# Kernel tuning notes

Measured on AMD Instinct MI355X. Metric: run time of the kernel, lower is better.

Reference implementation:

```python
import jax, jax.numpy as jnp
import numpy as np

B, S, D = 2, 2048, 1024
H, DK, DV = 16, 64, 64
NEG = -1e9

def setup_inputs() -> dict:
    key = jax.random.key(0)
    ks = jax.random.split(key, 7)
    scale = 1.0 / np.sqrt(D)
    return {
        "Q": jax.random.normal(ks[0], (B, S, D), dtype=jnp.float32),
        "K": jax.random.normal(ks[1], (B, S, D), dtype=jnp.float32),
        "V": jax.random.normal(ks[2], (B, S, D), dtype=jnp.float32),
        "Wq": jax.random.normal(ks[3], (D, H * DK), dtype=jnp.float32) * scale,
        "Wk": jax.random.normal(ks[4], (D, H * DK), dtype=jnp.float32) * scale,
        "Wv": jax.random.normal(ks[5], (D, H * DV), dtype=jnp.float32) * scale,
        "Wo": jax.random.normal(ks[6], (H * DV, D), dtype=jnp.float32) * scale,
    }

def reference(Q, K, V, Wq, Wk, Wv, Wo):
    b, sq, _ = Q.shape
    sk = K.shape[1]
    # project and split heads: [b, h, s, d]
    q = (Q @ Wq).reshape(b, sq, H, DK).transpose(0, 2, 1, 3)
    k = (K @ Wk).reshape(b, sk, H, DK).transpose(0, 2, 1, 3)
    v = (V @ Wv).reshape(b, sk, H, DV).transpose(0, 2, 1, 3)
    scores = jnp.einsum("bhqd,bhkd->bhqk", q, k) / jnp.sqrt(jnp.float32(DK))
    causal = jnp.tril(jnp.ones((sq, sk), dtype=bool))
    scores = jnp.where(causal[None, None], scores, NEG)
    attn = jax.nn.softmax(scores, axis=-1)
    out = jnp.einsum("bhqk,bhkd->bhqd", attn, v)
    out = out.transpose(0, 2, 1, 3).reshape(b, sq, H * DV)
    return out @ Wo
```

## Files before the change

kernel.cpp:

```cpp
#include <hip/hip_runtime.h>
#include <cstdint>
#include <cstddef>


typedef __bf16 bf16x8 __attribute__((ext_vector_type(8)));
typedef __bf16 bf16x4 __attribute__((ext_vector_type(4)));
typedef float f32x4 __attribute__((ext_vector_type(4)));
typedef unsigned int u32x4 __attribute__((ext_vector_type(4)));

#define MFMA __builtin_amdgcn_mfma_f32_16x16x32_bf16

static __device__ __forceinline__ __bf16 f2b(float f) { return (__bf16)f; }

static __device__ __forceinline__ void gload_lds16(const void* g, void* l) {
  __builtin_amdgcn_global_load_lds(
      (const __attribute__((address_space(1))) void*)g,
      (__attribute__((address_space(3))) void*)l, 16, 0, 0);
}

#define QSCALE 0.18033688f

__global__ __launch_bounds__(256) void wtrans_kernel(
    const float* __restrict__ w0, const float* __restrict__ w1,
    const float* __restrict__ w2, const float* __restrict__ w3,
    __bf16* __restrict__ outT)
{
  const int z = blockIdx.z;
  const float* W = (z == 0) ? w0 : (z == 1) ? w1 : (z == 2) ? w2 : w3;
  __bf16* O = outT + (size_t)z * 1048576;
  __shared__ float t[32][33];
  const int tx = threadIdx.x & 31, ty = threadIdx.x >> 5;
  const int kb = blockIdx.y * 32, nb = blockIdx.x * 32;
#pragma unroll
  for (int i = 0; i < 4; i++)
    t[ty + i * 8][tx] = W[(size_t)(kb + ty + i * 8) * 1024 + nb + tx];
  __syncthreads();
#pragma unroll
  for (int i = 0; i < 4; i++)
    O[(size_t)(nb + ty + i * 8) * 1024 + kb + tx] = f2b(t[tx][ty + i * 8]);
}

__global__ __launch_bounds__(256) void cvt_kernel(
    const float* __restrict__ a0, const float* __restrict__ a1,
    const float* __restrict__ a2, __bf16* __restrict__ o0,
    __bf16* __restrict__ o1, __bf16* __restrict__ o2)
{
  const int z = blockIdx.y;
  const float* src = (z == 0) ? a0 : (z == 1) ? a1 : a2;
  __bf16* dst = (z == 0) ? o0 : (z == 1) ? o1 : o2;
  const int idx = blockIdx.x * 256 + threadIdx.x;
#pragma unroll
  for (int it = 0; it < 4; ++it) {
    const size_t c = (size_t)(idx + it * 131072) * 8;
    f32x4 v0 = *(const f32x4*)&src[c];
    f32x4 v1 = *(const f32x4*)&src[c + 4];
    bf16x8 w = {f2b(v0[0]), f2b(v0[1]), f2b(v0[2]), f2b(v0[3]),
                f2b(v1[0]), f2b(v1[1]), f2b(v1[2]), f2b(v1[3])};
    *(bf16x8*)&dst[c] = w;
  }
}

__global__ __launch_bounds__(256) void gemm_proj_bf16_kernel(
    const __bf16* __restrict__ A0, const __bf16* __restrict__ A1,
    const __bf16* __restrict__ A2, const __bf16* __restrict__ WT,
    __bf16* __restrict__ C0, __bf16* __restrict__ C1, __bf16* __restrict__ C2)
{
  const int z = blockIdx.y;
  const __bf16* A = (z == 0) ? A0 : (z == 1) ? A1 : A2;
  const __bf16* W = WT + (size_t)z * 1048576;
  __bf16* C = (z == 0) ? C0 : (z == 1) ? C1 : C2;
  const float osc = (z == 0) ? QSCALE : 1.0f;

  const int bid = blockIdx.x;
  const int t = (bid & 7) * 32 + (bid >> 3);
  const int mt = t >> 3, nt = t & 7;
  const int mbase = mt * 128, nbase = nt * 128;

  __shared__ __align__(16) __bf16 As[128][32];
  __shared__ __align__(16) __bf16 Bs[128][32];

  const int tid = threadIdx.x;
  const int wid = tid >> 6, lane = tid & 63;
  const int wr = wid >> 1, wc = wid & 1;
  const int lr = lane & 15, kg = lane >> 4;

  f32x4 acc[4][4] = {};

  const int srow = tid >> 2, scol = (tid & 3) * 8;
  const int wbase = tid & 192;

  for (int kb = 0; kb < 32; ++kb) {
    const int k0 = kb * 32;
    __syncthreads();
#pragma unroll
    for (int p = 0; p < 2; ++p) {
      const int r = srow + p * 64;
      gload_lds16(&A[(size_t)(mbase + r) * 1024 + k0 + scol],
                  (__bf16*)As + (size_t)(p * 256 + wbase) * 8);
      gload_lds16(&W[(size_t)(nbase + r) * 1024 + k0 + scol],
                  (__bf16*)Bs + (size_t)(p * 256 + wbase) * 8);
    }
    __syncthreads();

    bf16x8 af[4], bfr[4];
#pragma unroll
    for (int i = 0; i < 4; i++) af[i] = *(const bf16x8*)&As[wr * 64 + i * 16 + lr][kg * 8];
#pragma unroll
    for (int j = 0; j < 4; j++) bfr[j] = *(const bf16x8*)&Bs[wc * 64 + j * 16 + lr][kg * 8];
#pragma unroll
    for (int i = 0; i < 4; i++)
#pragma unroll
      for (int j = 0; j < 4; j++)
        acc[i][j] = MFMA(af[i], bfr[j], acc[i][j], 0, 0, 0);
  }

  if (z == 2) {
#pragma unroll
    for (int i = 0; i < 4; i++)
#pragma unroll
      for (int j = 0; j < 4; j++) {
        const int m0 = mbase + wr * 64 + i * 16 + kg * 4;
        const int n = nbase + wc * 64 + j * 16 + lr;
        const int b = m0 >> 11, s = m0 & 2047, h = n >> 6, dv = n & 63;
        bf16x4 w;
#pragma unroll
        for (int r = 0; r < 4; r++) w[r] = f2b(acc[i][j][r]);
        *(bf16x4*)&C[(((size_t)(b * 16 + h)) * 64 + dv) * 2048 + s] = w;
      }
  } else {
#pragma unroll
    for (int i = 0; i < 4; i++)
#pragma unroll
      for (int j = 0; j < 4; j++)
#pragma unroll
        for (int r = 0; r < 4; r++) {
          const int m = mbase + wr * 64 + i * 16 + kg * 4 + r;
          const int n = nbase + wc * 64 + j * 16 + lr;
          const int b = m >> 11, s = m & 2047, h = n >> 6, dk = n & 63;
          C[(((size_t)(b * 16 + h)) * 2048 + s) * 64 + dk] = f2b(acc[i][j][r] * osc);
        }
  }
}

__global__ __launch_bounds__(256) void gemm_proj_f32_kernel(
    const float* __restrict__ A0, const float* __restrict__ A1,
    const float* __restrict__ A2, const __bf16* __restrict__ WT,
    __bf16* __restrict__ C0, __bf16* __restrict__ C1, __bf16* __restrict__ C2)
{
  const int z = blockIdx.y;
  const float* A = (z == 0) ? A0 : (z == 1) ? A1 : A2;
  const __bf16* W = WT + (size_t)z * 1048576;
  __bf16* C = (z == 0) ? C0 : (z == 1) ? C1 : C2;
  const float osc = (z == 0) ? QSCALE : 1.0f;

  const int mt = blockIdx.x >> 3, nt = blockIdx.x & 7;
  const int mbase = mt * 128, nbase = nt * 128;

  __shared__ __align__(16) __bf16 As[128][40];
  __shared__ __align__(16) __bf16 Bs[128][40];

  const int tid = threadIdx.x;
  const int wid = tid >> 6, lane = tid & 63;
  const int wr = wid >> 1, wc = wid & 1;
  const int lr = lane & 15, kg = lane >> 4;

  f32x4 acc[4][4] = {};
  const int arow = tid >> 3, ac0 = (tid & 7) * 4;

  for (int kb = 0; kb < 32; ++kb) {
    const int k0 = kb * 32;
#pragma unroll
    for (int p = 0; p < 4; ++p) {
      const int r = arow + p * 32;
      f32x4 av = *(const f32x4*)&A[(size_t)(mbase + r) * 1024 + k0 + ac0];
      bf16x4 cv = {f2b(av[0]), f2b(av[1]), f2b(av[2]), f2b(av[3])};
      *(bf16x4*)&As[r][ac0] = cv;
    }
#pragma unroll
    for (int p = 0; p < 2; ++p) {
      const int idx = p * 256 + tid;
      const int r = idx >> 2, c8 = (idx & 3) * 8;
      *(u32x4*)&Bs[r][c8] = *(const u32x4*)&W[(size_t)(nbase + r) * 1024 + k0 + c8];
    }
    __syncthreads();

    bf16x8 af[4], bfr[4];
#pragma unroll
    for (int i = 0; i < 4; i++) af[i] = *(const bf16x8*)&As[wr * 64 + i * 16 + lr][kg * 8];
#pragma unroll
    for (int j = 0; j < 4; j++) bfr[j] = *(const bf16x8*)&Bs[wc * 64 + j * 16 + lr][kg * 8];
#pragma unroll
    for (int i = 0; i < 4; i++)
#pragma unroll
      for (int j = 0; j < 4; j++)
        acc[i][j] = MFMA(af[i], bfr[j], acc[i][j], 0, 0, 0);
    __syncthreads();
  }

  if (z == 2) {
#pragma unroll
    for (int i = 0; i < 4; i++)
#pragma unroll
      for (int j = 0; j < 4; j++) {
        const int m0 = mbase + wr * 64 + i * 16 + kg * 4;
        const int n = nbase + wc * 64 + j * 16 + lr;
        const int b = m0 >> 11, s = m0 & 2047, h = n >> 6, dv = n & 63;
        bf16x4 w;
#pragma unroll
        for (int r = 0; r < 4; r++) w[r] = f2b(acc[i][j][r]);
        *(bf16x4*)&C[(((size_t)(b * 16 + h)) * 64 + dv) * 2048 + s] = w;
      }
  } else {
#pragma unroll
    for (int i = 0; i < 4; i++)
#pragma unroll
      for (int j = 0; j < 4; j++)
#pragma unroll
        for (int r = 0; r < 4; r++) {
          const int m = mbase + wr * 64 + i * 16 + kg * 4 + r;
          const int n = nbase + wc * 64 + j * 16 + lr;
          const int b = m >> 11, s = m & 2047, h = n >> 6, dk = n & 63;
          C[(((size_t)(b * 16 + h)) * 2048 + s) * 64 + dk] = f2b(acc[i][j][r] * osc);
        }
  }
}

__global__ __launch_bounds__(512) void attn_kernel(
    const __bf16* __restrict__ Qh, const __bf16* __restrict__ Kh,
    const __bf16* __restrict__ VTh, __bf16* __restrict__ AO)
{
  const int lin = blockIdx.x;
  const int l = (lin & 7) * 64 + (lin >> 3);
  const int bh = l >> 4;
  const int qblk = 15 - (l & 15);
  const int b = bh >> 4, h = bh & 15;
  const __bf16* Qp = Qh + (size_t)bh * 2048 * 64;
  const __bf16* Kp = Kh + (size_t)bh * 2048 * 64;
  const __bf16* Vp = VTh + (size_t)bh * 64 * 2048;

  __shared__ __align__(16) __bf16 Ks[2][64][72];
  __shared__ __align__(16) __bf16 Vt[2][64][72];
  __shared__ __align__(16) __bf16 Ps[8][16][72];

  const int tid = threadIdx.x, wid = tid >> 6, lane = tid & 63;
  const int lr = lane & 15, kg = lane >> 4;
  const int sr = tid >> 3, sc = (tid & 7) * 8;

  const int qbase = qblk << 7;
  const int nkv = 2 * qblk + 2;
  const int wq = qbase + wid * 16;

  bf16x8 qf0 = *(const bf16x8*)&Qp[(size_t)(wq + lr) * 64 + kg * 8];
  bf16x8 qf1 = *(const bf16x8*)&Qp[(size_t)(wq + lr) * 64 + 32 + kg * 8];

  f32x4 ot[4] = {};
  float mrow = -1e30f, lsum = 0.f;

  u32x4 kr = *(const u32x4*)&Kp[(size_t)sr * 64 + sc];
  u32x4 vr = *(const u32x4*)&Vp[(size_t)sr * 2048 + sc];
  *(u32x4*)&Ks[0][sr][sc] = kr;
  *(u32x4*)&Vt[0][sr][sc] = vr;

  int cur = 0;
  for (int t = 0; t < nkv; ++t) {
    const int kv0 = t << 6;
    const bool pre = (t + 1 < nkv);
    if (pre) {
      const int n0 = kv0 + 64;
      kr = *(const u32x4*)&Kp[(size_t)(n0 + sr) * 64 + sc];
      vr = *(const u32x4*)&Vp[(size_t)sr * 2048 + n0 + sc];
    }
    __syncthreads();

    if (kv0 <= wq + 15) {
      f32x4 st[4] = {};
      __builtin_amdgcn_s_setprio(1);
#pragma unroll
      for (int kvt = 0; kvt < 4; ++kvt) {
        bf16x8 kf0 = *(const bf16x8*)&Ks[cur][kvt * 16 + lr][kg * 8];
        bf16x8 kf1 = *(const bf16x8*)&Ks[cur][kvt * 16 + lr][32 + kg * 8];
        st[kvt] = MFMA(kf0, qf0, st[kvt], 0, 0, 0);
        st[kvt] = MFMA(kf1, qf1, st[kvt], 0, 0, 0);
      }
      __builtin_amdgcn_s_setprio(0);

      float sv[16];
#pragma unroll
      for (int kvt = 0; kvt < 4; ++kvt)
#pragma unroll
        for (int r = 0; r < 4; ++r) sv[kvt * 4 + r] = st[kvt][r];
      if (kv0 + 63 > wq) {
        const int qidx = wq + lr;
#pragma unroll
        for (int kvt = 0; kvt < 4; ++kvt)
#pragma unroll
          for (int r = 0; r < 4; ++r)
            if (kv0 + kvt * 16 + kg * 4 + r > qidx) sv[kvt * 4 + r] = -1e30f;
      }
      float mx = fmaxf(fmaxf(sv[0], sv[1]), sv[2]);
      mx = fmaxf(fmaxf(mx, sv[3]), sv[4]);
      mx = fmaxf(fmaxf(mx, sv[5]), sv[6]);
      mx = fmaxf(fmaxf(mx, sv[7]), sv[8]);
      mx = fmaxf(fmaxf(mx, sv[9]), sv[10]);
      mx = fmaxf(fmaxf(mx, sv[11]), sv[12]);
      mx = fmaxf(fmaxf(mx, sv[13]), sv[14]);
      mx = fmaxf(mx, sv[15]);
      mx = fmaxf(mx, __shfl_xor(mx, 16));
      mx = fmaxf(mx, __shfl_xor(mx, 32));
      if (__any(mx > mrow + 8.f)) {
        const float mnew = fmaxf(mrow, mx);
        const float scl = exp2f(mrow - mnew);
        mrow = mnew;
        lsum *= scl;
#pragma unroll
        for (int dvt = 0; dvt < 4; ++dvt) ot[dvt] *= scl;
      }
#pragma unroll
      for (int kvt = 0; kvt < 4; ++kvt) {
        bf16x4 pk;
#pragma unroll
        for (int r = 0; r < 4; ++r) {
          const float p = exp2f(sv[kvt * 4 + r] - mrow);
          lsum += p;
          pk[r] = f2b(p);
        }
        *(bf16x4*)&Ps[wid][lr][kvt * 16 + kg * 4] = pk;
      }

#pragma unroll
      for (int h2 = 0; h2 < 2; ++h2) {
        bf16x8 pf = *(const bf16x8*)&Ps[wid][lr][h2 * 32 + kg * 8];
        __builtin_amdgcn_s_setprio(1);
#pragma unroll
        for (int dvt = 0; dvt < 4; ++dvt) {
          bf16x8 vf = *(const bf16x8*)&Vt[cur][dvt * 16 + lr][h2 * 32 + kg * 8];
          ot[dvt] = MFMA(vf, pf, ot[dvt], 0, 0, 0);
        }
        __builtin_amdgcn_s_setprio(0);
      }
    }

    if (pre) {
      const int nb = cur ^ 1;
      *(u32x4*)&Ks[nb][sr][sc] = kr;
      *(u32x4*)&Vt[nb][sr][sc] = vr;
    }
    cur ^= 1;
  }

  lsum += __shfl_xor(lsum, 16);
  lsum += __shfl_xor(lsum, 32);
  const float rl = 1.f / lsum;
  const int q = wq + lr;
#pragma unroll
  for (int dvt = 0; dvt < 4; ++dvt) {
    bf16x4 w;
#pragma unroll
    for (int r = 0; r < 4; ++r) w[r] = f2b(ot[dvt][r] * rl);
    *(bf16x4*)&AO[((size_t)(b * 2048 + q)) * 1024 + h * 64 + dvt * 16 + kg * 4] = w;
  }
}

__global__ __launch_bounds__(256) void gemm_out_kernel(
    const __bf16* __restrict__ A, const __bf16* __restrict__ WT,
    float* __restrict__ Out)
{
  const int bid = blockIdx.x;
  const int t = (bid & 7) * 32 + (bid >> 3);
  const int mt = t >> 3, nt = t & 7;
  const int mbase = mt * 128, nbase = nt * 128;

  __shared__ __align__(16) __bf16 As[128][32];
  __shared__ __align__(16) __bf16 Bs[128][32];

  const int tid = threadIdx.x;
  const int wid = tid >> 6, lane = tid & 63;
  const int wr = wid >> 1, wc = wid & 1;
  const int lr = lane & 15, kg = lane >> 4;

  f32x4 acc[4][4] = {};

  const int srow = tid >> 2, scol = (tid & 3) * 8;
  const int wbase = tid & 192;

  for (int kb = 0; kb < 32; ++kb) {
    const int k0 = kb * 32;
    __syncthreads();
#pragma unroll
    for (int p = 0; p < 2; ++p) {
      const int r = srow + p * 64;
      gload_lds16(&A[(size_t)(mbase + r) * 1024 + k0 + scol],
                  (__bf16*)As + (size_t)(p * 256 + wbase) * 8);
      gload_lds16(&WT[(size_t)(nbase + r) * 1024 + k0 + scol],
                  (__bf16*)Bs + (size_t)(p * 256 + wbase) * 8);
    }
    __syncthreads();

    bf16x8 af[4], bfr[4];
#pragma unroll
    for (int i = 0; i < 4; i++) af[i] = *(const bf16x8*)&As[wr * 64 + i * 16 + lr][kg * 8];
#pragma unroll
    for (int j = 0; j < 4; j++) bfr[j] = *(const bf16x8*)&Bs[wc * 64 + j * 16 + lr][kg * 8];
#pragma unroll
    for (int i = 0; i < 4; i++)
#pragma unroll
      for (int j = 0; j < 4; j++)
        acc[i][j] = MFMA(af[i], bfr[j], acc[i][j], 0, 0, 0);
  }

#pragma unroll
  for (int i = 0; i < 4; i++)
#pragma unroll
    for (int j = 0; j < 4; j++)
#pragma unroll
      for (int r = 0; r < 4; r++) {
        const int m = mbase + wr * 64 + i * 16 + kg * 4 + r;
        const int n = nbase + wc * 64 + j * 16 + lr;
        Out[(size_t)m * 1024 + n] = acc[i][j][r];
      }
}

extern "C" void kernel_launch(void* const* d_in, const int* in_sizes, int n_in,
                              void* d_out, int out_size, void* d_ws, size_t ws_size,
                              hipStream_t stream) {
  const float* Q  = (const float*)d_in[0];
  const float* K  = (const float*)d_in[1];
  const float* V  = (const float*)d_in[2];
  const float* Wq = (const float*)d_in[3];
  const float* Wk = (const float*)d_in[4];
  const float* Wv = (const float*)d_in[5];
  const float* Wo = (const float*)d_in[6];
  float* out = (float*)d_out;

  const size_t M4 = 4194304;
  __bf16* wT  = (__bf16*)d_ws;
  __bf16* qb  = wT + M4;
  __bf16* kb  = qb + M4;
  __bf16* vtb = kb + M4;

  const bool fast = ws_size >= (size_t)(28 * 1048576) * 2;

  wtrans_kernel<<<dim3(32, 32, 4), 256, 0, stream>>>(Wq, Wk, Wv, Wo, wT);

  __bf16* ao;
  if (fast) {
    __bf16* qa = vtb + M4;
    __bf16* ka = qa + M4;
    __bf16* va = ka + M4;
    ao = qa;
    cvt_kernel<<<dim3(512, 3), 256, 0, stream>>>(Q, K, V, qa, ka, va);
    gemm_proj_bf16_kernel<<<dim3(256, 3), 256, 0, stream>>>(qa, ka, va, wT,
                                                            qb, kb, vtb);
  } else {
    ao = vtb + M4;
    gemm_proj_f32_kernel<<<dim3(256, 3), 256, 0, stream>>>(Q, K, V, wT,
                                                           qb, kb, vtb);
  }

  attn_kernel<<<dim3(512), 512, 0, stream>>>(qb, kb, vtb, ao);
  gemm_out_kernel<<<dim3(256), 256, 0, stream>>>(ao, wT + 3 * 1048576, out);
}
```

Measured before the change: 147.8 us.

## Use 4 waves each handling 32 query rows, with XOR-swizzled K/V LDS

The attention kernel moves from 8 waves of 16 query rows to 4 waves of 32 rows. Each K and V fragment read from LDS now feeds two query tiles, which halves LDS fragment traffic per MFMA. The K/V shared tiles drop their padding in favour of an XOR swizzle to avoid bank conflicts, and launch bounds are set to 256 threads with 3 blocks per CU. The cost is more registers per thread for the doubled accumulators and softmax state, and half as many waves per block to hide latency.

```diff
diff --git a/kernel.cpp b/kernel.cpp
--- a/kernel.cpp
+++ b/kernel.cpp
@@ -225,7 +225,7 @@
   }
 }
 
-__global__ __launch_bounds__(512) void attn_kernel(
+__global__ __launch_bounds__(256, 3) void attn_kernel(
     const __bf16* __restrict__ Qh, const __bf16* __restrict__ Kh,
     const __bf16* __restrict__ VTh, __bf16* __restrict__ AO)
 {
@@ -238,28 +238,39 @@
   const __bf16* Kp = Kh + (size_t)bh * 2048 * 64;
   const __bf16* Vp = VTh + (size_t)bh * 64 * 2048;
 
-  __shared__ __align__(16) __bf16 Ks[2][64][72];
-  __shared__ __align__(16) __bf16 Vt[2][64][72];
-  __shared__ __align__(16) __bf16 Ps[8][16][72];
+  __shared__ __align__(16) __bf16 Ks[2][64][64];
+  __shared__ __align__(16) __bf16 Vt[2][64][64];
+  __shared__ __align__(16) __bf16 Ps[4][32][72];
 
   const int tid = threadIdx.x, wid = tid >> 6, lane = tid & 63;
   const int lr = lane & 15, kg = lane >> 4;
-  const int sr = tid >> 3, sc = (tid & 7) * 8;
+  const int sr = tid >> 3, sg = tid & 7, sc0 = sg * 8;
+  const int swc = ((sg ^ (sr & 7)) << 3);
+  const int rs7 = lr & 7;
 
   const int qbase = qblk << 7;
   const int nkv = 2 * qblk + 2;
-  const int wq = qbase + wid * 16;
-
-  bf16x8 qf0 = *(const bf16x8*)&Qp[(size_t)(wq + lr) * 64 + kg * 8];
-  bf16x8 qf1 = *(const bf16x8*)&Qp[(size_t)(wq + lr) * 64 + 32 + kg * 8];
-
-  f32x4 ot[4] = {};
-  float mrow = -1e30f, lsum = 0.f;
-
-  u32x4 kr = *(const u32x4*)&Kp[(size_t)sr * 64 + sc];
-  u32x4 vr = *(const u32x4*)&Vp[(size_t)sr * 2048 + sc];
-  *(u32x4*)&Ks[0][sr][sc] = kr;
-  *(u32x4*)&Vt[0][sr][sc] = vr;
+  const int wq = qbase + wid * 32;
+
+  bf16x8 qf[2][2];
+#pragma unroll
+  for (int qt = 0; qt < 2; ++qt)
+#pragma unroll
+    for (int ks = 0; ks < 2; ++ks)
+      qf[qt][ks] = *(const bf16x8*)&Qp[(size_t)(wq + qt * 16 + lr) * 64 + ks * 32 + kg * 8];
+
+  f32x4 ot[2][4] = {};
+  float mrow[2] = {-1e30f, -1e30f};
+  float lsum[2] = {0.f, 0.f};
+
+  u32x4 kr0 = *(const u32x4*)&Kp[(size_t)sr * 64 + sc0];
+  u32x4 kr1 = *(const u32x4*)&Kp[(size_t)(sr + 32) * 64 + sc0];
+  u32x4 vr0 = *(const u32x4*)&Vp[(size_t)sr * 2048 + sc0];
+  u32x4 vr1 = *(const u32x4*)&Vp[(size_t)(sr + 32) * 2048 + sc0];
+  *(u32x4*)&Ks[0][sr][swc] = kr0;
+  *(u32x4*)&Ks[0][sr + 32][swc] = kr1;
+  *(u32x4*)&Vt[0][sr][swc] = vr0;
+  *(u32x4*)&Vt[0][sr + 32][swc] = vr1;
 
   int cur = 0;
   for (int t = 0; t < nkv; ++t) {
@@ -267,97 +278,119 @@
     const bool pre = (t + 1 < nkv);
     if (pre) {
       const int n0 = kv0 + 64;
-      kr = *(const u32x4*)&Kp[(size_t)(n0 + sr) * 64 + sc];
-      vr = *(const u32x4*)&Vp[(size_t)sr * 2048 + n0 + sc];
-    }
-    __syncthreads();
-
-    if (kv0 <= wq + 15) {
-      f32x4 st[4] = {};
+      kr0 = *(const u32x4*)&Kp[(size_t)(n0 + sr) * 64 + sc0];
+      kr1 = *(const u32x4*)&Kp[(size_t)(n0 + sr + 32) * 64 + sc0];
+      vr0 = *(const u32x4*)&Vp[(size_t)sr * 2048 + n0 + sc0];
+      vr1 = *(const u32x4*)&Vp[(size_t)(sr + 32) * 2048 + n0 + sc0];
+    }
+    __syncthreads();
+
+    if (kv0 <= wq + 31) {
+      f32x4 st[4][2] = {};
       __builtin_amdgcn_s_setprio(1);
 #pragma unroll
       for (int kvt = 0; kvt < 4; ++kvt) {
-        bf16x8 kf0 = *(const bf16x8*)&Ks[cur][kvt * 16 + lr][kg * 8];
-        bf16x8 kf1 = *(const bf16x8*)&Ks[cur][kvt * 16 + lr][32 + kg * 8];
-        st[kvt] = MFMA(kf0, qf0, st[kvt], 0, 0, 0);
-        st[kvt] = MFMA(kf1, qf1, st[kvt], 0, 0, 0);
+        const int row = kvt * 16 + lr;
+        bf16x8 kf0 = *(const bf16x8*)&Ks[cur][row][(kg ^ rs7) << 3];
+        bf16x8 kf1 = *(const bf16x8*)&Ks[cur][row][((4 + kg) ^ rs7) << 3];
+#pragma unroll
+        for (int qt = 0; qt < 2; ++qt) {
+          st[kvt][qt] = MFMA(kf0, qf[qt][0], st[kvt][qt], 0, 0, 0);
+          st[kvt][qt] = MFMA(kf1, qf[qt][1], st[kvt][qt], 0, 0, 0);
+        }
       }
       __builtin_amdgcn_s_setprio(0);
 
-      float sv[16];
-#pragma unroll
-      for (int kvt = 0; kvt < 4; ++kvt)
-#pragma unroll
-        for (int r = 0; r < 4; ++r) sv[kvt * 4 + r] = st[kvt][r];
-      if (kv0 + 63 > wq) {
-        const int qidx = wq + lr;
+#pragma unroll
+      for (int qt = 0; qt < 2; ++qt) {
+        float sv[16];
 #pragma unroll
         for (int kvt = 0; kvt < 4; ++kvt)
 #pragma unroll
-          for (int r = 0; r < 4; ++r)
-            if (kv0 + kvt * 16 + kg * 4 + r > qidx) sv[kvt * 4 + r] = -1e30f;
-      }
-      float mx = fmaxf(fmaxf(sv[0], sv[1]), sv[2]);
-      mx = fmaxf(fmaxf(mx, sv[3]), sv[4]);
-      mx = fmaxf(fmaxf(mx, sv[5]), sv[6]);
-      mx = fmaxf(fmaxf(mx, sv[7]), sv[8]);
-      mx = fmaxf(fmaxf(mx, sv[9]), sv[10]);
-      mx = fmaxf(fmaxf(mx, sv[11]), sv[12]);
-      mx = fmaxf(fmaxf(mx, sv[13]), sv[14]);
-      mx = fmaxf(mx, sv[15]);
-      mx = fmaxf(mx, __shfl_xor(mx, 16));
-      mx = fmaxf(mx, __shfl_xor(mx, 32));
-      if (__any(mx > mrow + 8.f)) {
-        const float mnew = fmaxf(mrow, mx);
-        const float scl = exp2f(mrow - mnew);
-        mrow = mnew;
-        lsum *= scl;
-#pragma unroll
-        for (int dvt = 0; dvt < 4; ++dvt) ot[dvt] *= scl;
-      }
-#pragma unroll
-      for (int kvt = 0; kvt < 4; ++kvt) {
-        bf16x4 pk;
-#pragma unroll
-        for (int r = 0; r < 4; ++r) {
-          const float p = exp2f(sv[kvt * 4 + r] - mrow);
-          lsum += p;
-          pk[r] = f2b(p);
-        }
-        *(bf16x4*)&Ps[wid][lr][kvt * 16 + kg * 4] = pk;
+          for (int r = 0; r < 4; ++r) sv[kvt * 4 + r] = st[kvt][qt][r];
+        if (kv0 + 63 > wq + qt * 16) {
+          const int qidx = wq + qt * 16 + lr;
+#pragma unroll
+          for (int kvt = 0; kvt < 4; ++kvt)
+#pragma unroll
+            for (int r = 0; r < 4; ++r)
+              if (kv0 + kvt * 16 + kg * 4 + r > qidx) sv[kvt * 4 + r] = -1e30f;
+        }
+        float mx = fmaxf(fmaxf(sv[0], sv[1]), sv[2]);
+        mx = fmaxf(fmaxf(mx, sv[3]), sv[4]);
+        mx = fmaxf(fmaxf(mx, sv[5]), sv[6]);
+        mx = fmaxf(fmaxf(mx, sv[7]), sv[8]);
+        mx = fmaxf(fmaxf(mx, sv[9]), sv[10]);
+        mx = fmaxf(fmaxf(mx, sv[11]), sv[12]);
+        mx = fmaxf(fmaxf(mx, sv[13]), sv[14]);
+        mx = fmaxf(mx, sv[15]);
+        mx = fmaxf(mx, __shfl_xor(mx, 16));
+        mx = fmaxf(mx, __shfl_xor(mx, 32));
+        if (__any(mx > mrow[qt] + 8.f)) {
+          const float mnew = fmaxf(mrow[qt], mx);
+          const float scl = exp2f(mrow[qt] - mnew);
+          mrow[qt] = mnew;
+          lsum[qt] *= scl;
+#pragma unroll
+          for (int dvt = 0; dvt < 4; ++dvt) ot[qt][dvt] *= scl;
+        }
+#pragma unroll
+        for (int kvt = 0; kvt < 4; ++kvt) {
+          bf16x4 pk;
+#pragma unroll
+          for (int r = 0; r < 4; ++r) {
+            const float p = exp2f(sv[kvt * 4 + r] - mrow[qt]);
+            lsum[qt] += p;
+            pk[r] = f2b(p);
+          }
+          *(bf16x4*)&Ps[wid][qt * 16 + lr][kvt * 16 + kg * 4] = pk;
+        }
       }
 
 #pragma unroll
       for (int h2 = 0; h2 < 2; ++h2) {
-        bf16x8 pf = *(const bf16x8*)&Ps[wid][lr][h2 * 32 + kg * 8];
-        __builtin_amdgcn_s_setprio(1);
+        bf16x8 vf[4];
 #pragma unroll
         for (int dvt = 0; dvt < 4; ++dvt) {
-          bf16x8 vf = *(const bf16x8*)&Vt[cur][dvt * 16 + lr][h2 * 32 + kg * 8];
-          ot[dvt] = MFMA(vf, pf, ot[dvt], 0, 0, 0);
-        }
-        __builtin_amdgcn_s_setprio(0);
+          const int row = dvt * 16 + lr;
+          vf[dvt] = *(const bf16x8*)&Vt[cur][row][((h2 * 4 + kg) ^ rs7) << 3];
+        }
+#pragma unroll
+        for (int qt = 0; qt < 2; ++qt) {
+          bf16x8 pf = *(const bf16x8*)&Ps[wid][qt * 16 + lr][h2 * 32 + kg * 8];
+          __builtin_amdgcn_s_setprio(1);
+#pragma unroll
+          for (int dvt = 0; dvt < 4; ++dvt)
+            ot[qt][dvt] = MFMA(vf[dvt], pf, ot[qt][dvt], 0, 0, 0);
+          __builtin_amdgcn_s_setprio(0);
+        }
       }
     }
 
     if (pre) {
       const int nb = cur ^ 1;
-      *(u32x4*)&Ks[nb][sr][sc] = kr;
-      *(u32x4*)&Vt[nb][sr][sc] = vr;
+      *(u32x4*)&Ks[nb][sr][swc] = kr0;
+      *(u32x4*)&Ks[nb][sr + 32][swc] = kr1;
+      *(u32x4*)&Vt[nb][sr][swc] = vr0;
+      *(u32x4*)&Vt[nb][sr + 32][swc] = vr1;
     }
     cur ^= 1;
   }
 
-  lsum += __shfl_xor(lsum, 16);
-  lsum += __shfl_xor(lsum, 32);
-  const float rl = 1.f / lsum;
-  const int q = wq + lr;
-#pragma unroll
-  for (int dvt = 0; dvt < 4; ++dvt) {
-    bf16x4 w;
-#pragma unroll
-    for (int r = 0; r < 4; ++r) w[r] = f2b(ot[dvt][r] * rl);
-    *(bf16x4*)&AO[((size_t)(b * 2048 + q)) * 1024 + h * 64 + dvt * 16 + kg * 4] = w;
+#pragma unroll
+  for (int qt = 0; qt < 2; ++qt) {
+    float ls = lsum[qt];
+    ls += __shfl_xor(ls, 16);
+    ls += __shfl_xor(ls, 32);
+    const float rl = 1.f / ls;
+    const int q = wq + qt * 16 + lr;
+#pragma unroll
+    for (int dvt = 0; dvt < 4; ++dvt) {
+      bf16x4 w;
+#pragma unroll
+      for (int r = 0; r < 4; ++r) w[r] = f2b(ot[qt][dvt][r] * rl);
+      *(bf16x4*)&AO[((size_t)(b * 2048 + q)) * 1024 + h * 64 + dvt * 16 + kg * 4] = w;
+    }
   }
 }
 
@@ -457,6 +490,6 @@
                                                            qb, kb, vtb);
   }
 
-  attn_kernel<<<dim3(512), 512, 0, stream>>>(qb, kb, vtb, ao);
+  attn_kernel<<<dim3(512), 256, 0, stream>>>(qb, kb, vtb, ao);
   gemm_out_kernel<<<dim3(256), 256, 0, stream>>>(ao, wT + 3 * 1048576, out);
 }
```

Result: slower. 150.8 us (+2.0%).
